# Performance work log

Measured on AMD Instinct MI355X. Metric: run time of the kernel, lower is better.

The kernel has to match this reference:

```python
import jax, jax.numpy as jnp
import numpy as np

HEADS = 4
HID = 32
IN = 128
OUT = 8
N = 50000
E = 1600000


def setup_inputs() -> dict:
    key = jax.random.key(0)
    ks = jax.random.split(key, 12)
    x = jax.random.normal(ks[0], (N, IN), dtype=jnp.float32)
    edge_index = jax.random.randint(ks[1], (2, E), 0, N, dtype=jnp.int64)
    s = 0.05
    W1 = jax.random.normal(ks[2], (IN, HEADS * HID), dtype=jnp.float32) * s
    att_src1 = jax.random.normal(ks[3], (HEADS, HID), dtype=jnp.float32) * s
    att_dst1 = jax.random.normal(ks[4], (HEADS, HID), dtype=jnp.float32) * s
    b1 = jnp.zeros((HEADS * HID,), dtype=jnp.float32)
    W2 = jax.random.normal(ks[5], (HEADS * HID, HEADS * HID), dtype=jnp.float32) * s
    att_src2 = jax.random.normal(ks[6], (HEADS, HID), dtype=jnp.float32) * s
    att_dst2 = jax.random.normal(ks[7], (HEADS, HID), dtype=jnp.float32) * s
    b2 = jnp.zeros((HEADS * HID,), dtype=jnp.float32)
    Wout = jax.random.normal(ks[8], (HEADS * HID, OUT), dtype=jnp.float32) * s
    bout = jnp.zeros((OUT,), dtype=jnp.float32)
    return {"x": x, "edge_index": edge_index, "W1": W1, "att_src1": att_src1,
            "att_dst1": att_dst1, "b1": b1, "W2": W2, "att_src2": att_src2,
            "att_dst2": att_dst2, "b2": b2, "Wout": Wout, "bout": bout}


def gat_conv(x, src, dst, W, att_src, att_dst, b):
    n = x.shape[0]
    h = (x @ W).reshape(n, HEADS, HID)              # [N,H,C]
    a_s = (h * att_src).sum(-1)                      # [N,H]
    a_d = (h * att_dst).sum(-1)                      # [N,H]
    e = jax.nn.leaky_relu(a_s[src] + a_d[dst], 0.2)  # [E,H]
    # scatter-softmax over incoming edges of each destination node
    m = jax.ops.segment_max(e, dst, num_segments=n)
    e = jnp.exp(e - m[dst])
    denom = jax.ops.segment_sum(e, dst, num_segments=n)
    alpha = e / (denom[dst] + 1e-16)                 # [E,H]
    msg = h[src] * alpha[:, :, None]                 # [E,H,C]
    out = jax.ops.segment_sum(msg, dst, num_segments=n)
    return out.reshape(n, HEADS * HID) + b


def reference(x, edge_index, W1, att_src1, att_dst1, b1, W2, att_src2, att_dst2, b2, Wout, bout):
    n = x.shape[0]
    # GATConv adds self-loops by default
    loops = jnp.arange(n, dtype=edge_index.dtype)
    src = jnp.concatenate([edge_index[0], loops])
    dst = jnp.concatenate([edge_index[1], loops])
    # dropout p=0.6 is identity in eval mode
    h = gat_conv(x, src, dst, W1, att_src1, att_dst1, b1)
    h = jax.nn.elu(h)
    h = gat_conv(h, src, dst, W2, att_src2, att_dst2, b2)
    return h @ Wout + bout
```

## Files before the change

### kernel.cpp

```cpp
#include <hip/hip_runtime.h>
#include <hip/hip_fp16.h>
#include <math.h>

#define N_NODES 50000
#define E_EDGES 1600000
#define NE_TOT  (E_EDGES + N_NODES)

#define BSH 7
#define NBKT ((N_NODES + 127) >> 7)
#define EPW 4096
#define NWA ((NE_TOT + EPW - 1) / EPW)
#define CAP 5120
#define CH 128


__device__ __forceinline__ void gemm_att_body(
    int bid, int t, float* Wl, float* xs,
    const float* __restrict__ X, const float* __restrict__ W,
    const float* __restrict__ attS, const float* __restrict__ attD,
    __half* __restrict__ H16, float* __restrict__ a_s, float* __restrict__ a_d) {
    int g = t >> 5, cl = t & 31, c4 = cl * 4;
    int rowbase = bid * 32;
    float4 acc[4];
    #pragma unroll
    for (int rr = 0; rr < 4; rr++) acc[rr] = make_float4(0.f, 0.f, 0.f, 0.f);

    for (int kp = 0; kp < 2; kp++) {
        __syncthreads();
        #pragma unroll
        for (int j = 0; j < 8; j++) {
            int f4 = t + 256 * j;
            int kk = f4 >> 5, cg2 = f4 & 31;
            *(float4*)&Wl[kk * 128 + cg2 * 4] =
                *(const float4*)&W[(kp * 64 + kk) * 128 + cg2 * 4];
        }
        #pragma unroll
        for (int j = 0; j < 2; j++) {
            int f4 = t + 256 * j;
            int r = f4 >> 4, k4 = f4 & 15;
            int grow = rowbase + r;
            float4 xv = make_float4(0.f, 0.f, 0.f, 0.f);
            if (grow < N_NODES) xv = *(const float4*)&X[grow * 128 + kp * 64 + k4 * 4];
            *(float4*)&xs[r * 64 + k4 * 4] = xv;
        }
        __syncthreads();
        #pragma unroll
        for (int k4 = 0; k4 < 16; k4++) {
            float4 xv[4];
            #pragma unroll
            for (int rr = 0; rr < 4; rr++)
                xv[rr] = *(float4*)&xs[(g * 4 + rr) * 64 + k4 * 4];
            #pragma unroll
            for (int kk = 0; kk < 4; kk++) {
                float4 wv = *(float4*)&Wl[(k4 * 4 + kk) * 128 + c4];
                #pragma unroll
                for (int rr = 0; rr < 4; rr++) {
                    float xc = (kk == 0) ? xv[rr].x : (kk == 1) ? xv[rr].y
                             : (kk == 2) ? xv[rr].z : xv[rr].w;
                    acc[rr].x += xc * wv.x;
                    acc[rr].y += xc * wv.y;
                    acc[rr].z += xc * wv.z;
                    acc[rr].w += xc * wv.w;
                }
            }
        }
    }

    float4 as4 = *(const float4*)&attS[c4];
    float4 ad4 = *(const float4*)&attD[c4];
    int head = cl >> 3;
    #pragma unroll
    for (int rr = 0; rr < 4; rr++) {
        int grow = rowbase + g * 4 + rr;
        float4 a = acc[rr];
        if (grow < N_NODES) {
            __half2 lo = __floats2half2_rn(a.x, a.y);
            __half2 hi = __floats2half2_rn(a.z, a.w);
            uint2 pk;
            pk.x = *(unsigned int*)&lo;
            pk.y = *(unsigned int*)&hi;
            *(uint2*)&H16[(size_t)grow * 128 + c4] = pk;
        }
        float ps = a.x * as4.x + a.y * as4.y + a.z * as4.z + a.w * as4.w;
        float pd = a.x * ad4.x + a.y * ad4.y + a.z * ad4.z + a.w * ad4.w;
        ps += __shfl_xor(ps, 1); ps += __shfl_xor(ps, 2); ps += __shfl_xor(ps, 4);
        pd += __shfl_xor(pd, 1); pd += __shfl_xor(pd, 2); pd += __shfl_xor(pd, 4);
        if ((cl & 7) == 0 && grow < N_NODES) {
            a_s[grow * 4 + head] = ps;
            a_d[grow * 4 + head] = pd;
        }
    }
}

__global__ __launch_bounds__(256) void k_hist_scatter_gemm(
    const int* __restrict__ ei, int* __restrict__ cursor,
    unsigned int* __restrict__ pairs,
    const float* __restrict__ X, const float* __restrict__ W,
    const float* __restrict__ attS, const float* __restrict__ attD,
    __half* __restrict__ H16, float* __restrict__ a_s, float* __restrict__ a_d) {
    __shared__ __align__(16) char smem[40960];
    int t = threadIdx.x;
    if (blockIdx.x < NWA) {
        int* h    = (int*)smem;
        int* wcur = ((int*)smem) + NBKT;
        for (int i = t; i < NBKT; i += 256) h[i] = 0;
        __syncthreads();
        int base = blockIdx.x * EPW;
        #pragma unroll 4
        for (int j = 0; j < EPW / 256; j++) {
            int e = base + t + 256 * j;
            if (e < NE_TOT) {
                int d = (e < E_EDGES) ? ei[E_EDGES + e] : (e - E_EDGES);
                atomicAdd(&h[d >> BSH], 1);
            }
        }
        __syncthreads();
        for (int i = t; i < NBKT; i += 256) {
            int c = h[i];
            int rel = (c > 0) ? atomicAdd(&cursor[i], c) : 0;
            wcur[i] = i * CAP + rel;
        }
        __syncthreads();
        #pragma unroll 4
        for (int j = 0; j < EPW / 256; j++) {
            int e = base + t + 256 * j;
            if (e < NE_TOT) {
                int s, d;
                if (e < E_EDGES) { s = ei[e]; d = ei[E_EDGES + e]; }
                else             { s = d = e - E_EDGES; }
                int pos = atomicAdd(&wcur[d >> BSH], 1);
                pairs[pos] = ((unsigned int)d << 16) | (unsigned int)s;
            }
        }
    } else {
        float* Wl = (float*)smem;
        float* xs = (float*)(smem + 32768);
        gemm_att_body(blockIdx.x - NWA, t, Wl, xs, X, W, attS, attD, H16, a_s, a_d);
    }
}

__global__ __launch_bounds__(256) void k_gemm_att(
    const float* __restrict__ X, const float* __restrict__ W,
    const float* __restrict__ attS, const float* __restrict__ attD,
    __half* __restrict__ H16, float* __restrict__ a_s, float* __restrict__ a_d) {
    __shared__ float Wl[64 * 128];
    __shared__ float xs[32 * 64];
    gemm_att_body(blockIdx.x, threadIdx.x, Wl, xs, X, W, attS, attD, H16, a_s, a_d);
}

__global__ __launch_bounds__(256) void k_bucketsort(
    const unsigned int* __restrict__ pairs, const int* __restrict__ cursor,
    int* __restrict__ rbeg, int* __restrict__ rend,
    unsigned short* __restrict__ col) {
    __shared__ int cnt[1 << BSH];
    __shared__ int sc[1 << BSH];
    __shared__ int cur[1 << BSH];
    int b = blockIdx.x, t = threadIdx.x;
    int nbeg = b << BSH;
    int ebeg = b * CAP;
    int eend = ebeg + cursor[b];
    if (t < (1 << BSH)) cnt[t] = 0;
    __syncthreads();
    for (int j = ebeg + t; j < eend; j += 256)
        atomicAdd(&cnt[(int)(pairs[j] >> 16) - nbeg], 1);
    __syncthreads();
    int v = (t < (1 << BSH)) ? cnt[t] : 0;
    if (t < (1 << BSH)) sc[t] = v;
    __syncthreads();
    for (int d = 1; d < (1 << BSH); d <<= 1) {
        int x = 0;
        if (t < (1 << BSH) && t >= d) x = sc[t - d];
        __syncthreads();
        if (t < (1 << BSH)) sc[t] += x;
        __syncthreads();
    }
    if (t < (1 << BSH)) {
        int pos = ebeg + sc[t] - v;
        cur[t] = pos;
        int node = nbeg + t;
        if (node < N_NODES) { rbeg[node] = pos; rend[node] = pos + v; }
    }
    __syncthreads();
    for (int j = ebeg + t; j < eend; j += 256) {
        unsigned int p = pairs[j];
        int pos = atomicAdd(&cur[(int)(p >> 16) - nbeg], 1);
        col[pos] = (unsigned short)(p & 0xFFFFu);
    }
}


__device__ inline float sel4(float4 v, int i) {
    float r = v.x;
    if (i == 1) r = v.y;
    if (i == 2) r = v.z;
    if (i == 3) r = v.w;
    return r;
}

__device__ inline float4 expleaky4(float4 a, float4 b) {
    float4 e, p;
    e.x = a.x + b.x; e.x = e.x > 0.f ? e.x : 0.2f * e.x; p.x = __expf(e.x);
    e.y = a.y + b.y; e.y = e.y > 0.f ? e.y : 0.2f * e.y; p.y = __expf(e.y);
    e.z = a.z + b.z; e.z = e.z > 0.f ? e.z : 0.2f * e.z; p.z = __expf(e.z);
    e.w = a.w + b.w; e.w = e.w > 0.f ? e.w : 0.2f * e.w; p.w = __expf(e.w);
    return p;
}

#define ACC8(q, raw)                                              \
    do {                                                          \
        const __half2* hp_ = (const __half2*)&(raw);              \
        float2 f0_ = __half22float2(hp_[0]);                      \
        float2 f1_ = __half22float2(hp_[1]);                      \
        float2 f2_ = __half22float2(hp_[2]);                      \
        float2 f3_ = __half22float2(hp_[3]);                      \
        acc8[0] = fmaf((q), f0_.x, acc8[0]);                      \
        acc8[1] = fmaf((q), f0_.y, acc8[1]);                      \
        acc8[2] = fmaf((q), f1_.x, acc8[2]);                      \
        acc8[3] = fmaf((q), f1_.y, acc8[3]);                      \
        acc8[4] = fmaf((q), f2_.x, acc8[4]);                      \
        acc8[5] = fmaf((q), f2_.y, acc8[5]);                      \
        acc8[6] = fmaf((q), f3_.x, acc8[6]);                      \
        acc8[7] = fmaf((q), f3_.y, acc8[7]);                      \
    } while (0)

template<int MODE>
__global__ __launch_bounds__(256) void k_agg(
    const __half* __restrict__ H16, const float* __restrict__ a_s,
    const float* __restrict__ a_d, const int* __restrict__ rbeg,
    const int* __restrict__ rend,
    const unsigned short* __restrict__ col, const float* __restrict__ bias,
    float* __restrict__ Hout,
    const float* __restrict__ Wout, const float* __restrict__ bout,
    float* __restrict__ out) {
    __shared__ float4 eS[4][CH];
    __shared__ int    sS[4][CH];
    __shared__ float  WoT[(MODE == 0) ? 1024 : 1];
    __shared__ float  boL[(MODE == 0) ? 8 : 1];

    if (MODE == 0) {
        for (int j = threadIdx.x; j < 1024; j += 256) {
            int o = j >> 7, k = j & 127;
            WoT[o * 128 + k] = Wout[k * 8 + o];
        }
        if (threadIdx.x < 8) boL[threadIdx.x] = bout[threadIdx.x];
        __syncthreads();
    }

    int wid = threadIdx.x >> 6;
    int lane = threadIdx.x & 63;
    int node = blockIdx.x * 4 + wid;
    if (node >= N_NODES) return;
    int beg = rbeg[node], end = rend[node];
    int deg = end - beg;
    float4 ad4 = *(const float4*)&a_d[node * 4];
    float4* eA = eS[wid];
    int*    srcA = sS[wid];

    float4 s = make_float4(0.f, 0.f, 0.f, 0.f);
    for (int j = beg + lane; j < end; j += 64) {
        int src = (int)col[j];
        float4 av = *(const float4*)&a_s[src * 4];
        float4 p = expleaky4(av, ad4);
        int idx = j - beg;
        if (idx < CH) { srcA[idx] = src; eA[idx] = p; }
        s.x += p.x; s.y += p.y; s.z += p.z; s.w += p.w;
    }
    #pragma unroll
    for (int off = 32; off > 0; off >>= 1) {
        s.x += __shfl_xor(s.x, off);
        s.y += __shfl_xor(s.y, off);
        s.z += __shfl_xor(s.z, off);
        s.w += __shfl_xor(s.w, off);
    }
    float4 inv;
    inv.x = 1.f / (s.x + 1e-16f);
    inv.y = 1.f / (s.y + 1e-16f);
    inv.z = 1.f / (s.z + 1e-16f);
    inv.w = 1.f / (s.w + 1e-16f);

    int eslot = lane >> 4, cl16 = lane & 15, head = cl16 >> 2;
    const __half* hbase = H16 + cl16 * 8;
    const float* pA = (const float*)eA;
    float acc8[8];
    #pragma unroll
    for (int k = 0; k < 8; k++) acc8[k] = 0.f;

    int nst = min(deg, CH);
    int i = eslot;
    for (; i + 12 < nst; i += 16) {
        int s0 = srcA[i];
        int s1 = srcA[i + 4];
        int s2 = srcA[i + 8];
        int s3 = srcA[i + 12];
        float q0 = pA[i * 4 + head];
        float q1 = pA[(i + 4) * 4 + head];
        float q2 = pA[(i + 8) * 4 + head];
        float q3 = pA[(i + 12) * 4 + head];
        float4 r0 = *(const float4*)(hbase + (size_t)s0 * 128);
        float4 r1 = *(const float4*)(hbase + (size_t)s1 * 128);
        float4 r2 = *(const float4*)(hbase + (size_t)s2 * 128);
        float4 r3 = *(const float4*)(hbase + (size_t)s3 * 128);
        ACC8(q0, r0);
        ACC8(q1, r1);
        ACC8(q2, r2);
        ACC8(q3, r3);
    }
    for (; i < nst; i += 4) {
        int src = srcA[i];
        float p = pA[i * 4 + head];
        float4 raw = *(const float4*)(hbase + (size_t)src * 128);
        ACC8(p, raw);
    }
    for (int cb = beg + CH; cb < end; cb += CH) {
        int cnt = min(end - cb, CH);
        for (int idx = lane; idx < cnt; idx += 64) {
            int src = (int)col[cb + idx];
            float4 av = *(const float4*)&a_s[src * 4];
            float4 p = expleaky4(av, ad4);
            srcA[idx] = src; eA[idx] = p;
        }
        for (int ii = eslot; ii < cnt; ii += 4) {
            int src = srcA[ii];
            float p = pA[ii * 4 + head];
            float4 raw = *(const float4*)(hbase + (size_t)src * 128);
            ACC8(p, raw);
        }
    }

    #pragma unroll
    for (int k = 0; k < 8; k++) {
        acc8[k] += __shfl_xor(acc8[k], 16);
        acc8[k] += __shfl_xor(acc8[k], 32);
    }

    float ih = sel4(inv, head);
    if (MODE == 1) {
        if (eslot == 0) {
            const float* bp = &bias[cl16 * 8];
            float o[8];
            #pragma unroll
            for (int k = 0; k < 8; k++) {
                o[k] = acc8[k] * ih + bp[k];
                o[k] = o[k] > 0.f ? o[k] : expm1f(o[k]);
            }
            float* op = &Hout[(size_t)node * 128 + cl16 * 8];
            *(float4*)&op[0] = make_float4(o[0], o[1], o[2], o[3]);
            *(float4*)&op[4] = make_float4(o[4], o[5], o[6], o[7]);
        }
    } else {
        const float* bp = &bias[cl16 * 8];
        float4 oa, ob;
        oa.x = acc8[0] * ih + bp[0]; oa.y = acc8[1] * ih + bp[1];
        oa.z = acc8[2] * ih + bp[2]; oa.w = acc8[3] * ih + bp[3];
        ob.x = acc8[4] * ih + bp[4]; ob.y = acc8[5] * ih + bp[5];
        ob.z = acc8[6] * ih + bp[6]; ob.w = acc8[7] * ih + bp[7];
        int o0 = eslot * 2;
        float p0 = 0.f, p1 = 0.f;
        {
            float4 wa = *(float4*)&WoT[o0 * 128 + cl16 * 8];
            float4 wb = *(float4*)&WoT[o0 * 128 + cl16 * 8 + 4];
            p0 = oa.x * wa.x + oa.y * wa.y + oa.z * wa.z + oa.w * wa.w
               + ob.x * wb.x + ob.y * wb.y + ob.z * wb.z + ob.w * wb.w;
            float4 wc = *(float4*)&WoT[(o0 + 1) * 128 + cl16 * 8];
            float4 wd = *(float4*)&WoT[(o0 + 1) * 128 + cl16 * 8 + 4];
            p1 = oa.x * wc.x + oa.y * wc.y + oa.z * wc.z + oa.w * wc.w
               + ob.x * wd.x + ob.y * wd.y + ob.z * wd.z + ob.w * wd.w;
        }
        #pragma unroll
        for (int d = 1; d <= 8; d <<= 1) {
            p0 += __shfl_xor(p0, d);
            p1 += __shfl_xor(p1, d);
        }
        if (cl16 == 0) {
            float2 ov = make_float2(p0 + boL[o0], p1 + boL[o0 + 1]);
            *(float2*)&out[(size_t)node * 8 + o0] = ov;
        }
    }
}


extern "C" void kernel_launch(void* const* d_in, const int* in_sizes, int n_in,
                              void* d_out, int out_size, void* d_ws, size_t ws_size,
                              hipStream_t stream) {
    const float* x     = (const float*)d_in[0];
    const int*   ei    = (const int*)d_in[1];
    const float* W1    = (const float*)d_in[2];
    const float* attS1 = (const float*)d_in[3];
    const float* attD1 = (const float*)d_in[4];
    const float* b1    = (const float*)d_in[5];
    const float* W2    = (const float*)d_in[6];
    const float* attS2 = (const float*)d_in[7];
    const float* attD2 = (const float*)d_in[8];
    const float* b2    = (const float*)d_in[9];
    const float* Wout  = (const float*)d_in[10];
    const float* bout  = (const float*)d_in[11];
    float* out = (float*)d_out;

    char* ws = (char*)d_ws;
    size_t off = 0;
    auto alloc = [&](size_t bytes) -> void* {
        void* p = ws + off;
        off += (bytes + 255) & ~(size_t)255;
        return p;
    };
    float*          hB     = (float*)alloc((size_t)N_NODES * 128 * 4);
    __half*         h16    = (__half*)alloc((size_t)N_NODES * 128 * 2);
    float*          a_s    = (float*)alloc((size_t)N_NODES * 4 * 4);
    float*          a_d    = (float*)alloc((size_t)N_NODES * 4 * 4);
    int*            rbeg   = (int*)alloc((size_t)N_NODES * 4);
    int*            rend   = (int*)alloc((size_t)N_NODES * 4);
    unsigned short* col    = (unsigned short*)alloc((size_t)NBKT * CAP * 2);
    int*            cursor = (int*)alloc((size_t)NBKT * 4);
    unsigned int*   pairs  = (unsigned int*)hB;

    int nbG = (N_NODES + 31) / 32;
    int nbA = (N_NODES + 3) / 4;

    hipMemsetAsync(cursor, 0, (size_t)NBKT * 4, stream);
    k_hist_scatter_gemm<<<NWA + nbG, 256, 0, stream>>>(
        ei, cursor, pairs, x, W1, attS1, attD1, h16, a_s, a_d);
    k_bucketsort<<<NBKT, 256, 0, stream>>>(pairs, cursor, rbeg, rend, col);

    k_agg<1><<<nbA, 256, 0, stream>>>(h16, a_s, a_d, rbeg, rend, col, b1, hB,
                                      Wout, bout, out);
    k_gemm_att<<<nbG, 256, 0, stream>>>(hB, W2, attS2, attD2, h16, a_s, a_d);
    k_agg<0><<<nbA, 256, 0, stream>>>(h16, a_s, a_d, rbeg, rend, col, b2, hB,
                                      Wout, bout, out);
}
```

Measured before the change: 253.9 us.

## Use fp16 MFMA for node-feature GEMM with 64-row tiles

Replaces the scalar fp32 FMA GEMM in the feature transform plus attention-logit kernel with 16x16x32 fp16 MFMA instructions. X and W are converted to fp16 in padded LDS tiles, and each block now handles 64 rows instead of 32. Attention logits are reduced from the accumulator fragments with lane shuffles. The aim is to cut ALU time in both GEMM launches, at the cost of fp16 input rounding, a strided scalar LDS gather for the B fragment, and scalar 2-byte H16 stores.

```diff
diff --git a/kernel.cpp b/kernel.cpp
--- a/kernel.cpp
+++ b/kernel.cpp
@@ -13,82 +13,128 @@
 #define CAP 5120
 #define CH 128
 
+#define GROWS 64
+#define XH_STRIDE 136
+#define WR_STRIDE 130
+#define XH_BYTES (GROWS * XH_STRIDE * 2)
+#define WR_BYTES (128 * WR_STRIDE * 2)
+#define GEMM_LDS (XH_BYTES + WR_BYTES)
+
+typedef _Float16 f16x8 __attribute__((ext_vector_type(8)));
+typedef float    f32x4 __attribute__((ext_vector_type(4)));
+
 
 __device__ __forceinline__ void gemm_att_body(
-    int bid, int t, float* Wl, float* xs,
+    int bid, int t, _Float16* xh, _Float16* wr,
     const float* __restrict__ X, const float* __restrict__ W,
     const float* __restrict__ attS, const float* __restrict__ attD,
     __half* __restrict__ H16, float* __restrict__ a_s, float* __restrict__ a_d) {
-    int g = t >> 5, cl = t & 31, c4 = cl * 4;
-    int rowbase = bid * 32;
-    float4 acc[4];
-    #pragma unroll
-    for (int rr = 0; rr < 4; rr++) acc[rr] = make_float4(0.f, 0.f, 0.f, 0.f);
-
-    for (int kp = 0; kp < 2; kp++) {
-        __syncthreads();
-        #pragma unroll
-        for (int j = 0; j < 8; j++) {
-            int f4 = t + 256 * j;
-            int kk = f4 >> 5, cg2 = f4 & 31;
-            *(float4*)&Wl[kk * 128 + cg2 * 4] =
-                *(const float4*)&W[(kp * 64 + kk) * 128 + cg2 * 4];
-        }
-        #pragma unroll
-        for (int j = 0; j < 2; j++) {
-            int f4 = t + 256 * j;
-            int r = f4 >> 4, k4 = f4 & 15;
-            int grow = rowbase + r;
-            float4 xv = make_float4(0.f, 0.f, 0.f, 0.f);
-            if (grow < N_NODES) xv = *(const float4*)&X[grow * 128 + kp * 64 + k4 * 4];
-            *(float4*)&xs[r * 64 + k4 * 4] = xv;
-        }
-        __syncthreads();
-        #pragma unroll
-        for (int k4 = 0; k4 < 16; k4++) {
-            float4 xv[4];
-            #pragma unroll
-            for (int rr = 0; rr < 4; rr++)
-                xv[rr] = *(float4*)&xs[(g * 4 + rr) * 64 + k4 * 4];
-            #pragma unroll
-            for (int kk = 0; kk < 4; kk++) {
-                float4 wv = *(float4*)&Wl[(k4 * 4 + kk) * 128 + c4];
-                #pragma unroll
-                for (int rr = 0; rr < 4; rr++) {
-                    float xc = (kk == 0) ? xv[rr].x : (kk == 1) ? xv[rr].y
-                             : (kk == 2) ? xv[rr].z : xv[rr].w;
-                    acc[rr].x += xc * wv.x;
-                    acc[rr].y += xc * wv.y;
-                    acc[rr].z += xc * wv.z;
-                    acc[rr].w += xc * wv.w;
+    int rowbase = bid * GROWS;
+
+    #pragma unroll
+    for (int j = 0; j < 8; j++) {
+        int f4 = t + 256 * j;
+        int r  = f4 >> 5;
+        int k4 = (f4 & 31) * 4;
+        int grow = rowbase + r;
+        float4 xv = make_float4(0.f, 0.f, 0.f, 0.f);
+        if (grow < N_NODES) xv = *(const float4*)&X[(size_t)grow * 128 + k4];
+        __half2 lo = __floats2half2_rn(xv.x, xv.y);
+        __half2 hi = __floats2half2_rn(xv.z, xv.w);
+        *(__half2*)&xh[r * XH_STRIDE + k4]     = lo;
+        *(__half2*)&xh[r * XH_STRIDE + k4 + 2] = hi;
+    }
+    #pragma unroll
+    for (int j = 0; j < 16; j++) {
+        int f4 = t + 256 * j;
+        int k  = f4 >> 5;
+        int c0 = (f4 & 31) * 4;
+        float4 wv = *(const float4*)&W[k * 128 + c0];
+        __half2 lo = __floats2half2_rn(wv.x, wv.y);
+        __half2 hi = __floats2half2_rn(wv.z, wv.w);
+        *(__half2*)&wr[k * WR_STRIDE + c0]     = lo;
+        *(__half2*)&wr[k * WR_STRIDE + c0 + 2] = hi;
+    }
+    __syncthreads();
+
+    int lane = t & 63;
+    int w    = t >> 6;
+    int lrow = lane & 15;
+    int g    = lane >> 4;
+
+    f16x8 afr[4][4];
+    #pragma unroll
+    for (int rt = 0; rt < 4; rt++)
+        #pragma unroll
+        for (int ks = 0; ks < 4; ks++)
+            afr[rt][ks] = *(f16x8*)&xh[(rt * 16 + lrow) * XH_STRIDE + ks * 32 + g * 8];
+
+    f32x4 acc[2][4];
+    #pragma unroll
+    for (int hf = 0; hf < 2; hf++)
+        #pragma unroll
+        for (int rt = 0; rt < 4; rt++)
+            acc[hf][rt] = (f32x4){0.f, 0.f, 0.f, 0.f};
+
+    #pragma unroll
+    for (int hf = 0; hf < 2; hf++) {
+        int c = (w * 2 + hf) * 16 + lrow;
+        #pragma unroll
+        for (int ks = 0; ks < 4; ks++) {
+            f16x8 bfr;
+            #pragma unroll
+            for (int j = 0; j < 8; j++)
+                bfr[j] = wr[(ks * 32 + g * 8 + j) * WR_STRIDE + c];
+            #pragma unroll
+            for (int rt = 0; rt < 4; rt++)
+                acc[hf][rt] = __builtin_amdgcn_mfma_f32_16x16x32_f16(
+                    afr[rt][ks], bfr, acc[hf][rt], 0, 0, 0);
+        }
+    }
+
+    float ps[4][4], pd[4][4];
+    #pragma unroll
+    for (int rt = 0; rt < 4; rt++)
+        #pragma unroll
+        for (int r = 0; r < 4; r++) { ps[rt][r] = 0.f; pd[rt][r] = 0.f; }
+
+    #pragma unroll
+    for (int hf = 0; hf < 2; hf++) {
+        int ch = (w * 2 + hf) * 16 + lrow;
+        float aS = attS[ch], aD = attD[ch];
+        #pragma unroll
+        for (int rt = 0; rt < 4; rt++) {
+            #pragma unroll
+            for (int r = 0; r < 4; r++) {
+                float v = acc[hf][rt][r];
+                int grow = rowbase + rt * 16 + g * 4 + r;
+                if (grow < N_NODES) H16[(size_t)grow * 128 + ch] = __float2half(v);
+                ps[rt][r] = fmaf(v, aS, ps[rt][r]);
+                pd[rt][r] = fmaf(v, aD, pd[rt][r]);
+            }
+        }
+    }
+    #pragma unroll
+    for (int rt = 0; rt < 4; rt++)
+        #pragma unroll
+        for (int r = 0; r < 4; r++) {
+            #pragma unroll
+            for (int d = 1; d <= 8; d <<= 1) {
+                ps[rt][r] += __shfl_xor(ps[rt][r], d);
+                pd[rt][r] += __shfl_xor(pd[rt][r], d);
+            }
+        }
+    if (lrow == 0) {
+        #pragma unroll
+        for (int rt = 0; rt < 4; rt++)
+            #pragma unroll
+            for (int r = 0; r < 4; r++) {
+                int grow = rowbase + rt * 16 + g * 4 + r;
+                if (grow < N_NODES) {
+                    a_s[grow * 4 + w] = ps[rt][r];
+                    a_d[grow * 4 + w] = pd[rt][r];
                 }
             }
-        }
-    }
-
-    float4 as4 = *(const float4*)&attS[c4];
-    float4 ad4 = *(const float4*)&attD[c4];
-    int head = cl >> 3;
-    #pragma unroll
-    for (int rr = 0; rr < 4; rr++) {
-        int grow = rowbase + g * 4 + rr;
-        float4 a = acc[rr];
-        if (grow < N_NODES) {
-            __half2 lo = __floats2half2_rn(a.x, a.y);
-            __half2 hi = __floats2half2_rn(a.z, a.w);
-            uint2 pk;
-            pk.x = *(unsigned int*)&lo;
-            pk.y = *(unsigned int*)&hi;
-            *(uint2*)&H16[(size_t)grow * 128 + c4] = pk;
-        }
-        float ps = a.x * as4.x + a.y * as4.y + a.z * as4.z + a.w * as4.w;
-        float pd = a.x * ad4.x + a.y * ad4.y + a.z * ad4.z + a.w * ad4.w;
-        ps += __shfl_xor(ps, 1); ps += __shfl_xor(ps, 2); ps += __shfl_xor(ps, 4);
-        pd += __shfl_xor(pd, 1); pd += __shfl_xor(pd, 2); pd += __shfl_xor(pd, 4);
-        if ((cl & 7) == 0 && grow < N_NODES) {
-            a_s[grow * 4 + head] = ps;
-            a_d[grow * 4 + head] = pd;
-        }
     }
 }
 
@@ -98,7 +144,7 @@
     const float* __restrict__ X, const float* __restrict__ W,
     const float* __restrict__ attS, const float* __restrict__ attD,
     __half* __restrict__ H16, float* __restrict__ a_s, float* __restrict__ a_d) {
-    __shared__ __align__(16) char smem[40960];
+    __shared__ __align__(16) char smem[GEMM_LDS];
     int t = threadIdx.x;
     if (blockIdx.x < NWA) {
         int* h    = (int*)smem;
@@ -133,9 +179,9 @@
             }
         }
     } else {
-        float* Wl = (float*)smem;
-        float* xs = (float*)(smem + 32768);
-        gemm_att_body(blockIdx.x - NWA, t, Wl, xs, X, W, attS, attD, H16, a_s, a_d);
+        _Float16* xh = (_Float16*)smem;
+        _Float16* wr = (_Float16*)(smem + XH_BYTES);
+        gemm_att_body(blockIdx.x - NWA, t, xh, wr, X, W, attS, attD, H16, a_s, a_d);
     }
 }
 
@@ -143,9 +189,10 @@
     const float* __restrict__ X, const float* __restrict__ W,
     const float* __restrict__ attS, const float* __restrict__ attD,
     __half* __restrict__ H16, float* __restrict__ a_s, float* __restrict__ a_d) {
-    __shared__ float Wl[64 * 128];
-    __shared__ float xs[32 * 64];
-    gemm_att_body(blockIdx.x, threadIdx.x, Wl, xs, X, W, attS, attD, H16, a_s, a_d);
+    __shared__ __align__(16) char smem[GEMM_LDS];
+    _Float16* xh = (_Float16*)smem;
+    _Float16* wr = (_Float16*)(smem + XH_BYTES);
+    gemm_att_body(blockIdx.x, threadIdx.x, xh, wr, X, W, attS, attD, H16, a_s, a_d);
 }
 
 __global__ __launch_bounds__(256) void k_bucketsort(
@@ -413,7 +460,7 @@
     int*            cursor = (int*)alloc((size_t)NBKT * 4);
     unsigned int*   pairs  = (unsigned int*)hB;
 
-    int nbG = (N_NODES + 31) / 32;
+    int nbG = (N_NODES + GROWS - 1) / GROWS;
     int nbA = (N_NODES + 3) / 4;
 
     hipMemsetAsync(cursor, 0, (size_t)NBKT * 4, stream);
```

After: 236.3 us. -6.9%, faster.
